# Performance work log

Measured on AMD Instinct MI355X. Metric: run time of the kernel, lower is better.

Reference implementation:

```python
import jax, jax.numpy as jnp
import numpy as np

VOCAB = 50257
HIDDEN = 1024
BATCH = 4
SEQ = 4096

def setup_inputs() -> dict:
    key = jax.random.key(0)
    k_idx, k_w = jax.random.split(key)
    idx = jax.random.randint(k_idx, (BATCH, SEQ), 0, VOCAB, dtype=jnp.int64 if jax.config.jax_enable_x64 else jnp.int32)
    weight = jax.random.normal(k_w, (VOCAB, HIDDEN), dtype=jnp.float32)
    return {"idx": idx, "weight": weight}

def reference(idx, weight):
    # Equivalent to the SUMMA loop: for each vocab partition i, build a masked
    # one-hot matrix and addmm into the output; summed over partitions this is
    # exactly a full-vocab embedding gather.
    # idx: (B, S) int; weight: (VOCAB, HIDDEN)
    return jnp.take(weight, idx, axis=0)  # (B, S, HIDDEN)
```

## Files before the change

kernel.cpp:

```cpp
#include <hip/hip_runtime.h>
#include <hip/hip_bf16.h>


#define HIDDEN 1024
#define VEC4_PER_ROW (HIDDEN / 4)

__global__ __launch_bounds__(256) void embed_gather_kernel(
    const int* __restrict__ idx,
    const float* __restrict__ weight,
    float* __restrict__ out)
{
    const int token = blockIdx.x;
    const int row = idx[token];

    const float4* __restrict__ src =
        reinterpret_cast<const float4*>(weight + (size_t)row * HIDDEN);
    float4* __restrict__ dst =
        reinterpret_cast<float4*>(out + (size_t)token * HIDDEN);

    dst[threadIdx.x] = src[threadIdx.x];
}

extern "C" void kernel_launch(void* const* d_in, const int* in_sizes, int n_in,
                              void* d_out, int out_size, void* d_ws, size_t ws_size,
                              hipStream_t stream) {
    const int* idx = (const int*)d_in[0];
    const float* weight = (const float*)d_in[1];
    float* out = (float*)d_out;

    const int n_tokens = in_sizes[0];

    embed_gather_kernel<<<n_tokens, 256, 0, stream>>>(idx, weight, out);
}
```

Measured before the change: 268.9 us.

## Batch eight tokens per block and use nontemporal stores for gathered rows

Each block now handles eight tokens instead of one, issuing all eight row loads before any stores so more memory requests are in flight per thread. Output writes use nontemporal stores to avoid polluting cache with the write-only output. The grid shrinks eightfold and register use per thread rises, which could reduce the available parallelism.

```diff
diff --git a/kernel.cpp b/kernel.cpp
--- a/kernel.cpp
+++ b/kernel.cpp
@@ -3,22 +3,41 @@
 
 
 #define HIDDEN 1024
-#define VEC4_PER_ROW (HIDDEN / 4)
+#define TOKENS_PER_BLOCK 8
+
+typedef float f32x4 __attribute__((ext_vector_type(4)));
 
 __global__ __launch_bounds__(256) void embed_gather_kernel(
     const int* __restrict__ idx,
     const float* __restrict__ weight,
-    float* __restrict__ out)
+    float* __restrict__ out,
+    int n_tokens)
 {
-    const int token = blockIdx.x;
-    const int row = idx[token];
+    const int t0 = blockIdx.x * TOKENS_PER_BLOCK;
+    const int lane = threadIdx.x;
 
-    const float4* __restrict__ src =
-        reinterpret_cast<const float4*>(weight + (size_t)row * HIDDEN);
-    float4* __restrict__ dst =
-        reinterpret_cast<float4*>(out + (size_t)token * HIDDEN);
+    f32x4 v[TOKENS_PER_BLOCK];
 
-    dst[threadIdx.x] = src[threadIdx.x];
+    #pragma unroll
+    for (int t = 0; t < TOKENS_PER_BLOCK; ++t) {
+        const int tok = t0 + t;
+        if (tok < n_tokens) {
+            const int row = idx[tok];
+            const f32x4* __restrict__ src =
+                reinterpret_cast<const f32x4*>(weight + (size_t)row * HIDDEN);
+            v[t] = src[lane];
+        }
+    }
+
+    #pragma unroll
+    for (int t = 0; t < TOKENS_PER_BLOCK; ++t) {
+        const int tok = t0 + t;
+        if (tok < n_tokens) {
+            f32x4* __restrict__ dst =
+                reinterpret_cast<f32x4*>(out + (size_t)tok * HIDDEN);
+            __builtin_nontemporal_store(v[t], dst + lane);
+        }
+    }
 }
 
 extern "C" void kernel_launch(void* const* d_in, const int* in_sizes, int n_in,
@@ -29,6 +48,7 @@
     float* out = (float*)d_out;
 
     const int n_tokens = in_sizes[0];
+    const int n_blocks = (n_tokens + TOKENS_PER_BLOCK - 1) / TOKENS_PER_BLOCK;
 
-    embed_gather_kernel<<<n_tokens, 256, 0, stream>>>(idx, weight, out);
+    embed_gather_kernel<<<n_blocks, 256, 0, stream>>>(idx, weight, out, n_tokens);
 }
```

Result: slower. 276.4 us (+2.8%).
